# Performance work log

Hardware: AMD Instinct MI355X
Metric: run time of the kernel (lower is better)

Reference implementation:

```python
import jax, jax.numpy as jnp
import numpy as np

HIDDEN = 512
N_DRUG = 2000
N_REACTION = 10000
N_EDGES = 400000


def setup_inputs() -> dict:
    key = jax.random.key(0)
    ks = jax.random.split(key, 6)
    z_drug = jax.random.normal(ks[0], (N_DRUG, HIDDEN), dtype=jnp.float32)
    z_reaction = jax.random.normal(ks[1], (N_REACTION, HIDDEN), dtype=jnp.float32)
    row = jax.random.randint(ks[2], (N_EDGES,), 0, N_DRUG, dtype=jnp.int64)
    col = jax.random.randint(ks[3], (N_EDGES,), 0, N_REACTION, dtype=jnp.int64)
    # Linear weights in torch layout: (out_features, in_features)
    W1 = jax.random.normal(ks[4], (HIDDEN, 2 * HIDDEN), dtype=jnp.float32) * (1.0 / np.sqrt(2 * HIDDEN))
    b1 = jnp.zeros((HIDDEN,), dtype=jnp.float32)
    W2 = jax.random.normal(ks[5], (1, HIDDEN), dtype=jnp.float32) * (1.0 / np.sqrt(HIDDEN))
    b2 = jnp.zeros((1,), dtype=jnp.float32)
    return {"z_drug": z_drug, "z_reaction": z_reaction, "row": row, "col": col,
            "W1": W1, "b1": b1, "W2": W2, "b2": b2}


def reference(z_drug, z_reaction, row, col, W1, b1, W2, b2):
    # gather + concat: [E, 2H]
    z = jnp.concatenate([z_drug[row], z_reaction[col]], axis=-1)
    h = jax.nn.relu(jnp.einsum('eh,oh->eo', z, W1) + b1)  # [E, H]
    out = jnp.einsum('eh,oh->eo', h, W2) + b2             # [E, 1]
    return out.reshape(-1)
```

## Files before the change

### kernel.cpp

```cpp
#include <hip/hip_runtime.h>
#include <stdint.h>

#define HIDDEN 512
#define NDRUG 2000
#define NREACT 10000
#define NEDGE 400000

#define NBKT 320
#define SLOT 2048
#define CSTRIDE 16
#define NSCAT 128
#define EPB ((NEDGE + NSCAT - 1) / NSCAT)

#define BPB2 2
#define EBLK (NBKT * BPB2)
#define MAXSL 1024
#define HRSTRIDE 520
#define ETHREADS 512

#define GEMMBLKS 380

typedef __attribute__((ext_vector_type(8))) _Float16 f16x8;
typedef __attribute__((ext_vector_type(2))) _Float16 f16x2;
typedef __attribute__((ext_vector_type(4))) float f32x4;
typedef __attribute__((ext_vector_type(4))) float float4v;
typedef __attribute__((ext_vector_type(4))) _Float16 f16x4;

#if defined(__has_builtin)
#if __has_builtin(__builtin_amdgcn_fdot2)
#define HAVE_FDOT2 1
#endif
#endif

__global__ __launch_bounds__(256) void prep_kernel(
    const float* __restrict__ z_drug, const float* __restrict__ z_react,
    const float* __restrict__ W1,
    _Float16* __restrict__ zd_f, _Float16* __restrict__ zr_f,
    _Float16* __restrict__ WL, _Float16* __restrict__ WR,
    int* __restrict__ cursor)
{
  const int b = blockIdx.x;
  const int tid = threadIdx.x;
  if (b < 128) {
    const int nth = 128 * 256;
    const int NQ = NDRUG * HIDDEN / 4;
    for (int i = b * 256 + tid; i < NQ; i += nth) {
      float4v v = *reinterpret_cast<const float4v*>(z_drug + (size_t)i * 4);
      f16x4 q; q[0]=(_Float16)v[0]; q[1]=(_Float16)v[1]; q[2]=(_Float16)v[2]; q[3]=(_Float16)v[3];
      *reinterpret_cast<f16x4*>(zd_f + (size_t)i * 4) = q;
    }
  } else if (b < 768) {
    const int nth = 640 * 256;
    const int NQ = NREACT * HIDDEN / 4;
    for (int i = (b - 128) * 256 + tid; i < NQ; i += nth) {
      float4v v = *reinterpret_cast<const float4v*>(z_react + (size_t)i * 4);
      f16x4 q; q[0]=(_Float16)v[0]; q[1]=(_Float16)v[1]; q[2]=(_Float16)v[2]; q[3]=(_Float16)v[3];
      *reinterpret_cast<f16x4*>(zr_f + (size_t)i * 4) = q;
    }
  } else if (b < 1024) {
    const int nth = 256 * 256;
    const int NQ = HIDDEN * 2 * HIDDEN / 4;
    for (int i = (b - 768) * 256 + tid; i < NQ; i += nth) {
      int e = i * 4;
      int o = e >> 10, j = e & 1023;
      float4v v = *reinterpret_cast<const float4v*>(W1 + e);
      f16x4 q; q[0]=(_Float16)v[0]; q[1]=(_Float16)v[1]; q[2]=(_Float16)v[2]; q[3]=(_Float16)v[3];
      if (j < HIDDEN) *reinterpret_cast<f16x4*>(WL + o * HIDDEN + j) = q;
      else            *reinterpret_cast<f16x4*>(WR + o * HIDDEN + (j - HIDDEN)) = q;
    }
  } else {
    int i = (b - 1024) * 256 + tid;
    if (i < NBKT) cursor[i * CSTRIDE] = i * SLOT;
  }
}

#define BM 128
#define BN 128
#define BK 32

__global__ __launch_bounds__(256) void gemm_scatter(
    const _Float16* __restrict__ Adrug, const _Float16* __restrict__ Areac,
    const _Float16* __restrict__ BL, const _Float16* __restrict__ BR,
    const float* __restrict__ bias,
    const int* __restrict__ row, const int* __restrict__ col,
    _Float16* __restrict__ Hd, _Float16* __restrict__ Hr,
    int* __restrict__ cursor, uint64_t* __restrict__ pk)
{
  __shared__ _Float16 As[BM * BK];
  __shared__ _Float16 Bs[BN * BK];
  __shared__ int lhist[NBKT];
  __shared__ int lbase[NBKT];

  const int bid = blockIdx.x;
  const int tid = threadIdx.x;

  if (bid >= GEMMBLKS) {
    const int sb = bid - GEMMBLKS;
    const int e0 = sb * EPB;
    const int e1 = (e0 + EPB < NEDGE) ? e0 + EPB : NEDGE;
    for (int i = tid; i < NBKT; i += 256) lhist[i] = 0;
    __syncthreads();
    for (int e = e0 + tid; e < e1; e += 256)
      atomicAdd(&lhist[col[e] >> 5], 1);
    __syncthreads();
    for (int i = tid; i < NBKT; i += 256) {
      int cnt = lhist[i];
      lbase[i] = cnt ? atomicAdd(&cursor[i * CSTRIDE], cnt) : 0;
      lhist[i] = 0;
    }
    __syncthreads();
    for (int e = e0 + tid; e < e1; e += 256) {
      int c = col[e];
      int r = row[e];
      int bkt = c >> 5;
      int lo = atomicAdd(&lhist[bkt], 1);
      pk[lbase[bkt] + lo] = ((uint64_t)e << 25) | ((uint64_t)r << 14) | (uint64_t)c;
    }
    return;
  }

  const int z = (bid >= 64) ? 1 : 0;
  const int t = z ? bid - 64 : bid;
  const int mb = t >> 2;
  const int nb = t & 3;
  const int M = (z == 0) ? NDRUG : NREACT;
  const _Float16* A = (z == 0) ? Adrug : Areac;
  const _Float16* B = (z == 0) ? BL : BR;
  _Float16* C = (z == 0) ? Hd : Hr;
  const bool has_bias = (z == 0);
  const int K = HIDDEN, N = HIDDEN;

  const int lane = tid & 63;
  const int wid = tid >> 6;
  const int wm = wid >> 1;
  const int wn = wid & 1;

  f32x4 acc[4][4];
#pragma unroll
  for (int i = 0; i < 4; ++i)
#pragma unroll
    for (int j = 0; j < 4; ++j) acc[i][j] = (f32x4){0.f, 0.f, 0.f, 0.f};

  const int row0 = mb * BM;
  const int col0 = nb * BN;
  const int srow = lane >> 2;
  const int scol = (lane & 3) * 8;

  for (int kt = 0; kt < K; kt += BK) {
#pragma unroll
    for (int i = 0; i < 2; ++i) {
      int rA = row0 + wid * 32 + i * 16 + srow;
      rA = rA < M ? rA : M - 1;
      const _Float16* gA = A + (size_t)rA * K + kt + scol;
      _Float16* lA = As + (wid * 32 + i * 16) * BK;
      __builtin_amdgcn_global_load_lds(
          (const __attribute__((address_space(1))) void*)gA,
          (__attribute__((address_space(3))) void*)lA, 16, 0, 0);
      int rB = col0 + wid * 32 + i * 16 + srow;
      const _Float16* gB = B + (size_t)rB * K + kt + scol;
      _Float16* lB = Bs + (wid * 32 + i * 16) * BK;
      __builtin_amdgcn_global_load_lds(
          (const __attribute__((address_space(1))) void*)gB,
          (__attribute__((address_space(3))) void*)lB, 16, 0, 0);
    }
    __syncthreads();

    const int fr = lane & 15;
    const int kg = (lane >> 4) * 8;
    f16x8 af[4], bfr[4];
#pragma unroll
    for (int mi = 0; mi < 4; ++mi)
      af[mi] = *reinterpret_cast<const f16x8*>(As + (wm * 64 + mi * 16 + fr) * BK + kg);
#pragma unroll
    for (int ni = 0; ni < 4; ++ni)
      bfr[ni] = *reinterpret_cast<const f16x8*>(Bs + (wn * 64 + ni * 16 + fr) * BK + kg);
#pragma unroll
    for (int mi = 0; mi < 4; ++mi)
#pragma unroll
      for (int ni = 0; ni < 4; ++ni)
        acc[mi][ni] = __builtin_amdgcn_mfma_f32_16x16x32_f16(af[mi], bfr[ni], acc[mi][ni], 0, 0, 0);
    __syncthreads();
  }

  const int crow = (lane >> 4) * 4;
  const int ccol = lane & 15;
#pragma unroll
  for (int ni = 0; ni < 4; ++ni) {
    const int gc = col0 + wn * 64 + ni * 16 + ccol;
    const float bv = has_bias ? bias[gc] : 0.0f;
#pragma unroll
    for (int mi = 0; mi < 4; ++mi) {
#pragma unroll
      for (int j = 0; j < 4; ++j) {
        const int gr = row0 + wm * 64 + mi * 16 + crow + j;
        if (gr < M) C[(size_t)gr * N + gc] = (_Float16)(acc[mi][ni][j] + bv);
      }
    }
  }
}

__global__ __launch_bounds__(ETHREADS) void edge_kernel(
    const _Float16* __restrict__ Hd, const _Float16* __restrict__ Hr,
    const uint64_t* __restrict__ pk, const int* __restrict__ cursor,
    const float* __restrict__ W2, const float* __restrict__ b2,
    float* __restrict__ out)
{
  __shared__ _Float16 hrs[32 * HRSTRIDE];
  __shared__ uint64_t raw[MAXSL];
  __shared__ uint64_t spk[MAXSL];
  __shared__ int qdesc[MAXSL / 4 + 32];
  __shared__ int cnt[32], cb[32], cnt2[32], qoff[32];
  __shared__ int nqs;

  const int bid = blockIdx.x;
  const int xcd = bid & 7;
  const int idx = bid >> 3;
  const int bucket = xcd * 40 + (idx >> 1);
  const int slice = idx & 1;
  const int base = bucket * SLOT;
  const int count = cursor[bucket * CSTRIDE] - base;
  const int per = (count + BPB2 - 1) / BPB2;
  const int s = slice * per;
  const int e_end0 = (s + per < count) ? s + per : count;
  const int n = (e_end0 > s) ? e_end0 - s : 0;

  const int tid = threadIdx.x;
  const int lane = tid & 63;
  const int li = lane & 15;
  const int wv = tid >> 6;
  const int gid = wv * 4 + (lane >> 4);

#pragma unroll
  for (int rr2 = 0; rr2 < 4; ++rr2) {
    int rr = wv * 4 + rr2;
    int gr = bucket * 32 + rr;
    gr = (gr < NREACT) ? gr : NREACT - 1;
    const _Float16* src = Hr + (size_t)gr * HIDDEN + lane * 8;
    _Float16* dst = hrs + rr * HRSTRIDE;
    __builtin_amdgcn_global_load_lds(
        (const __attribute__((address_space(1))) void*)src,
        (__attribute__((address_space(3))) void*)dst, 16, 0, 0);
  }

  f16x8 w2v[4];
#pragma unroll
  for (int k = 0; k < 4; ++k) {
    const float* p = W2 + li * 8 + k * 128;
    f16x8 q;
#pragma unroll
    for (int j = 0; j < 8; ++j) q[j] = (_Float16)p[j];
    w2v[k] = q;
  }
  const float bias2 = *b2;
  const f16x8 zero8 = (f16x8)(_Float16)0;

  if (tid < 32) { cnt[tid] = 0; cnt2[tid] = 0; }
  __syncthreads();
  for (int i = tid; i < n; i += ETHREADS) {
    uint64_t p = pk[base + s + i];
    raw[i] = p;
    atomicAdd(&cnt[(int)(p & 31)], 1);
  }
  __syncthreads();
  if (tid == 0) {
    int acc = 0, qa = 0;
    for (int j = 0; j < 32; ++j) {
      cb[j] = acc; acc += cnt[j];
      qoff[j] = qa; qa += (cnt[j] + 3) >> 2;
    }
    nqs = qa;
  }
  __syncthreads();
  for (int i = tid; i < n; i += ETHREADS) {
    uint64_t p = raw[i];
    int lc = (int)(p & 31);
    int lo = atomicAdd(&cnt2[lc], 1);
    spk[cb[lc] + lo] = p;
  }
  __syncthreads();
  if (tid < 32) {
    int j = tid, st = cb[j], len = cnt[j], o = qoff[j];
    for (int q = 0; q < len; q += 4) {
      int cn = len - q; cn = (cn < 4) ? cn : 4;
      qdesc[o++] = j | ((st + q) << 5) | (cn << 16);
    }
  }
  __syncthreads();

  const int nq = nqs;
  for (int q = gid; q < nq; q += 32) {
    const int d = qdesc[q];
    const int lc = d & 31;
    const int st = (d >> 5) & 2047;
    const int cn = (d >> 16) & 7;

    const _Float16* hd[4];
    int si[4];
#pragma unroll
    for (int j = 0; j < 4; ++j) {
      int jj = (j < cn) ? j : cn - 1;
      uint64_t p = spk[st + jj];
      si[j] = (int)(p >> 25);
      hd[j] = Hd + (size_t)((p >> 14) & 0x7FF) * HIDDEN;
    }

    f16x8 vd[4][4];
#pragma unroll
    for (int j = 0; j < 4; ++j)
#pragma unroll
      for (int k = 0; k < 4; ++k)
        vd[j][k] = *reinterpret_cast<const f16x8*>(hd[j] + li * 8 + k * 128);

    f16x8 hv[4];
#pragma unroll
    for (int k = 0; k < 4; ++k)
      hv[k] = *reinterpret_cast<const f16x8*>(hrs + lc * HRSTRIDE + li * 8 + k * 128);

    float acc[4] = {0.f, 0.f, 0.f, 0.f};
#pragma unroll
    for (int j = 0; j < 4; ++j) {
#pragma unroll
      for (int k = 0; k < 4; ++k) {
        f16x8 t = __builtin_elementwise_max(vd[j][k] + hv[k], zero8);
#if defined(HAVE_FDOT2)
#pragma unroll
        for (int qq = 0; qq < 4; ++qq) {
          f16x2 wp = {w2v[k][2 * qq], w2v[k][2 * qq + 1]};
          f16x2 sp = {t[2 * qq], t[2 * qq + 1]};
          acc[j] = __builtin_amdgcn_fdot2(sp, wp, acc[j], false);
        }
#else
#pragma unroll
        for (int qq = 0; qq < 8; ++qq)
          acc[j] += (float)t[qq] * (float)w2v[k][qq];
#endif
      }
    }
#pragma unroll
    for (int off = 8; off >= 1; off >>= 1) {
#pragma unroll
      for (int j = 0; j < 4; ++j) acc[j] += __shfl_xor(acc[j], off);
    }
    if (li == 0) {
      for (int j = 0; j < cn; ++j) out[si[j]] = acc[j] + bias2;
    }
  }
}

extern "C" void kernel_launch(void* const* d_in, const int* in_sizes, int n_in,
                              void* d_out, int out_size, void* d_ws, size_t ws_size,
                              hipStream_t stream) {
  const float* z_drug  = (const float*)d_in[0];
  const float* z_react = (const float*)d_in[1];
  const int*   row     = (const int*)d_in[2];
  const int*   col     = (const int*)d_in[3];
  const float* W1      = (const float*)d_in[4];
  const float* b1      = (const float*)d_in[5];
  const float* W2      = (const float*)d_in[6];
  const float* b2      = (const float*)d_in[7];
  float* out = (float*)d_out;

  char* ws = (char*)d_ws;
  size_t off = 0;
  auto alloc = [&](size_t bytes) {
    void* p = ws + off;
    off += (bytes + 255) & ~(size_t)255;
    return p;
  };
  _Float16* zd_f = (_Float16*)alloc((size_t)NDRUG * HIDDEN * 2);
  _Float16* zr_f = (_Float16*)alloc((size_t)NREACT * HIDDEN * 2);
  _Float16* wl_f = (_Float16*)alloc((size_t)HIDDEN * HIDDEN * 2);
  _Float16* wr_f = (_Float16*)alloc((size_t)HIDDEN * HIDDEN * 2);
  _Float16* Hd   = (_Float16*)alloc((size_t)NDRUG * HIDDEN * 2);
  _Float16* Hr   = (_Float16*)alloc((size_t)NREACT * HIDDEN * 2);
  int*      cursor = (int*)alloc((size_t)NBKT * CSTRIDE * 4);
  uint64_t* pk     = (uint64_t*)alloc((size_t)NBKT * SLOT * 8);

  prep_kernel<<<1026, 256, 0, stream>>>(z_drug, z_react, W1,
                                        zd_f, zr_f, wl_f, wr_f, cursor);
  gemm_scatter<<<GEMMBLKS + NSCAT, 256, 0, stream>>>(zd_f, zr_f, wl_f, wr_f, b1,
                                                     row, col, Hd, Hr, cursor, pk);
  edge_kernel<<<EBLK, ETHREADS, 0, stream>>>(Hd, Hr, pk, cursor, W2, b2, out);
}
```

Measured before the change: 67.47 us.

## Fuse fp32-to-fp16 conversion into GEMM LDS loads, drop prep kernel

Removes the separate prep kernel that converted z_drug, z_reaction and W1 to fp16 in global memory. The GEMM now loads fp32 tiles straight into LDS and converts to fp16 when building the MFMA fragments, reading W1 in place with a column offset. This saves a full read/write pass over the embeddings and one kernel launch, at the cost of doubling LDS tile size and global load traffic inside the GEMM, plus conversion work in the inner loop.

```diff
diff --git a/kernel.cpp b/kernel.cpp
--- a/kernel.cpp
+++ b/kernel.cpp
@@ -23,8 +23,8 @@
 typedef __attribute__((ext_vector_type(8))) _Float16 f16x8;
 typedef __attribute__((ext_vector_type(2))) _Float16 f16x2;
 typedef __attribute__((ext_vector_type(4))) float f32x4;
+typedef __attribute__((ext_vector_type(8))) float f32x8;
 typedef __attribute__((ext_vector_type(4))) float float4v;
-typedef __attribute__((ext_vector_type(4))) _Float16 f16x4;
 
 #if defined(__has_builtin)
 #if __has_builtin(__builtin_amdgcn_fdot2)
@@ -32,46 +32,9 @@
 #endif
 #endif
 
-__global__ __launch_bounds__(256) void prep_kernel(
-    const float* __restrict__ z_drug, const float* __restrict__ z_react,
-    const float* __restrict__ W1,
-    _Float16* __restrict__ zd_f, _Float16* __restrict__ zr_f,
-    _Float16* __restrict__ WL, _Float16* __restrict__ WR,
-    int* __restrict__ cursor)
-{
-  const int b = blockIdx.x;
-  const int tid = threadIdx.x;
-  if (b < 128) {
-    const int nth = 128 * 256;
-    const int NQ = NDRUG * HIDDEN / 4;
-    for (int i = b * 256 + tid; i < NQ; i += nth) {
-      float4v v = *reinterpret_cast<const float4v*>(z_drug + (size_t)i * 4);
-      f16x4 q; q[0]=(_Float16)v[0]; q[1]=(_Float16)v[1]; q[2]=(_Float16)v[2]; q[3]=(_Float16)v[3];
-      *reinterpret_cast<f16x4*>(zd_f + (size_t)i * 4) = q;
-    }
-  } else if (b < 768) {
-    const int nth = 640 * 256;
-    const int NQ = NREACT * HIDDEN / 4;
-    for (int i = (b - 128) * 256 + tid; i < NQ; i += nth) {
-      float4v v = *reinterpret_cast<const float4v*>(z_react + (size_t)i * 4);
-      f16x4 q; q[0]=(_Float16)v[0]; q[1]=(_Float16)v[1]; q[2]=(_Float16)v[2]; q[3]=(_Float16)v[3];
-      *reinterpret_cast<f16x4*>(zr_f + (size_t)i * 4) = q;
-    }
-  } else if (b < 1024) {
-    const int nth = 256 * 256;
-    const int NQ = HIDDEN * 2 * HIDDEN / 4;
-    for (int i = (b - 768) * 256 + tid; i < NQ; i += nth) {
-      int e = i * 4;
-      int o = e >> 10, j = e & 1023;
-      float4v v = *reinterpret_cast<const float4v*>(W1 + e);
-      f16x4 q; q[0]=(_Float16)v[0]; q[1]=(_Float16)v[1]; q[2]=(_Float16)v[2]; q[3]=(_Float16)v[3];
-      if (j < HIDDEN) *reinterpret_cast<f16x4*>(WL + o * HIDDEN + j) = q;
-      else            *reinterpret_cast<f16x4*>(WR + o * HIDDEN + (j - HIDDEN)) = q;
-    }
-  } else {
-    int i = (b - 1024) * 256 + tid;
-    if (i < NBKT) cursor[i * CSTRIDE] = i * SLOT;
-  }
+__global__ __launch_bounds__(256) void init_cursor(int* __restrict__ cursor) {
+  int i = blockIdx.x * blockDim.x + threadIdx.x;
+  if (i < NBKT) cursor[i * CSTRIDE] = i * SLOT;
 }
 
 #define BM 128
@@ -79,15 +42,15 @@
 #define BK 32
 
 __global__ __launch_bounds__(256) void gemm_scatter(
-    const _Float16* __restrict__ Adrug, const _Float16* __restrict__ Areac,
-    const _Float16* __restrict__ BL, const _Float16* __restrict__ BR,
+    const float* __restrict__ z_drug, const float* __restrict__ z_react,
+    const float* __restrict__ W1,
     const float* __restrict__ bias,
     const int* __restrict__ row, const int* __restrict__ col,
     _Float16* __restrict__ Hd, _Float16* __restrict__ Hr,
     int* __restrict__ cursor, uint64_t* __restrict__ pk)
 {
-  __shared__ _Float16 As[BM * BK];
-  __shared__ _Float16 Bs[BN * BK];
+  __shared__ float As[BM * BK];
+  __shared__ float Bs[BN * BK];
   __shared__ int lhist[NBKT];
   __shared__ int lbase[NBKT];
 
@@ -124,8 +87,8 @@
   const int mb = t >> 2;
   const int nb = t & 3;
   const int M = (z == 0) ? NDRUG : NREACT;
-  const _Float16* A = (z == 0) ? Adrug : Areac;
-  const _Float16* B = (z == 0) ? BL : BR;
+  const float* A = (z == 0) ? z_drug : z_react;
+  const int boff = (z == 0) ? 0 : HIDDEN;
   _Float16* C = (z == 0) ? Hd : Hr;
   const bool has_bias = (z == 0);
   const int K = HIDDEN, N = HIDDEN;
@@ -143,22 +106,22 @@
 
   const int row0 = mb * BM;
   const int col0 = nb * BN;
-  const int srow = lane >> 2;
-  const int scol = (lane & 3) * 8;
+  const int srow8 = lane >> 3;
+  const int scol4 = (lane & 7) * 4;
 
   for (int kt = 0; kt < K; kt += BK) {
 #pragma unroll
-    for (int i = 0; i < 2; ++i) {
-      int rA = row0 + wid * 32 + i * 16 + srow;
+    for (int i = 0; i < 4; ++i) {
+      int rA = row0 + wid * 32 + i * 8 + srow8;
       rA = rA < M ? rA : M - 1;
-      const _Float16* gA = A + (size_t)rA * K + kt + scol;
-      _Float16* lA = As + (wid * 32 + i * 16) * BK;
+      const float* gA = A + (size_t)rA * K + kt + scol4;
+      float* lA = As + (wid * 32 + i * 8) * BK;
       __builtin_amdgcn_global_load_lds(
           (const __attribute__((address_space(1))) void*)gA,
           (__attribute__((address_space(3))) void*)lA, 16, 0, 0);
-      int rB = col0 + wid * 32 + i * 16 + srow;
-      const _Float16* gB = B + (size_t)rB * K + kt + scol;
-      _Float16* lB = Bs + (wid * 32 + i * 16) * BK;
+      int rB = col0 + wid * 32 + i * 8 + srow8;
+      const float* gB = W1 + (size_t)rB * (2 * HIDDEN) + boff + kt + scol4;
+      float* lB = Bs + (wid * 32 + i * 8) * BK;
       __builtin_amdgcn_global_load_lds(
           (const __attribute__((address_space(1))) void*)gB,
           (__attribute__((address_space(3))) void*)lB, 16, 0, 0);
@@ -169,11 +132,15 @@
     const int kg = (lane >> 4) * 8;
     f16x8 af[4], bfr[4];
 #pragma unroll
-    for (int mi = 0; mi < 4; ++mi)
-      af[mi] = *reinterpret_cast<const f16x8*>(As + (wm * 64 + mi * 16 + fr) * BK + kg);
-#pragma unroll
-    for (int ni = 0; ni < 4; ++ni)
-      bfr[ni] = *reinterpret_cast<const f16x8*>(Bs + (wn * 64 + ni * 16 + fr) * BK + kg);
+    for (int mi = 0; mi < 4; ++mi) {
+      f32x8 v = *reinterpret_cast<const f32x8*>(As + (wm * 64 + mi * 16 + fr) * BK + kg);
+      af[mi] = __builtin_convertvector(v, f16x8);
+    }
+#pragma unroll
+    for (int ni = 0; ni < 4; ++ni) {
+      f32x8 v = *reinterpret_cast<const f32x8*>(Bs + (wn * 64 + ni * 16 + fr) * BK + kg);
+      bfr[ni] = __builtin_convertvector(v, f16x8);
+    }
 #pragma unroll
     for (int mi = 0; mi < 4; ++mi)
 #pragma unroll
@@ -367,18 +334,13 @@
     off += (bytes + 255) & ~(size_t)255;
     return p;
   };
-  _Float16* zd_f = (_Float16*)alloc((size_t)NDRUG * HIDDEN * 2);
-  _Float16* zr_f = (_Float16*)alloc((size_t)NREACT * HIDDEN * 2);
-  _Float16* wl_f = (_Float16*)alloc((size_t)HIDDEN * HIDDEN * 2);
-  _Float16* wr_f = (_Float16*)alloc((size_t)HIDDEN * HIDDEN * 2);
   _Float16* Hd   = (_Float16*)alloc((size_t)NDRUG * HIDDEN * 2);
   _Float16* Hr   = (_Float16*)alloc((size_t)NREACT * HIDDEN * 2);
   int*      cursor = (int*)alloc((size_t)NBKT * CSTRIDE * 4);
   uint64_t* pk     = (uint64_t*)alloc((size_t)NBKT * SLOT * 8);
 
-  prep_kernel<<<1026, 256, 0, stream>>>(z_drug, z_react, W1,
-                                        zd_f, zr_f, wl_f, wr_f, cursor);
-  gemm_scatter<<<GEMMBLKS + NSCAT, 256, 0, stream>>>(zd_f, zr_f, wl_f, wr_f, b1,
+  init_cursor<<<2, 256, 0, stream>>>(cursor);
+  gemm_scatter<<<GEMMBLKS + NSCAT, 256, 0, stream>>>(z_drug, z_react, W1, b1,
                                                      row, col, Hd, Hr, cursor, pk);
   edge_kernel<<<EBLK, ETHREADS, 0, stream>>>(Hd, Hr, pk, cursor, W2, b2, out);
 }
```

Result: slower. 76.39 us (+13.2%).

## Fuse fp32-to-fp16 activation conversion into GEMM and split edge buckets four ways

Applied to the files above, without the earlier changes.

Removes the separate conversion pass for z_drug and z_reaction. The GEMM now loads fp32 rows directly, converts them to fp16 in registers and stores them to LDS, so the fp16 copies are no longer written to and re-read from global memory. The edge kernel splits each bucket into four slices instead of two, which doubles the block count and halves the per-block LDS staging buffers. Risks include a weaker A-tile load path (register staging instead of direct-to-LDS), a changed barrier pattern, and MAXSL 512 possibly overflowing if a bucket slice exceeds 512 edges.

```diff
diff --git a/kernel.cpp b/kernel.cpp
--- a/kernel.cpp
+++ b/kernel.cpp
@@ -12,9 +12,9 @@
 #define NSCAT 128
 #define EPB ((NEDGE + NSCAT - 1) / NSCAT)
 
-#define BPB2 2
+#define BPB2 4
 #define EBLK (NBKT * BPB2)
-#define MAXSL 1024
+#define MAXSL 512
 #define HRSTRIDE 520
 #define ETHREADS 512
 
@@ -23,6 +23,7 @@
 typedef __attribute__((ext_vector_type(8))) _Float16 f16x8;
 typedef __attribute__((ext_vector_type(2))) _Float16 f16x2;
 typedef __attribute__((ext_vector_type(4))) float f32x4;
+typedef __attribute__((ext_vector_type(8))) float f32x8;
 typedef __attribute__((ext_vector_type(4))) float float4v;
 typedef __attribute__((ext_vector_type(4))) _Float16 f16x4;
 
@@ -32,35 +33,16 @@
 #endif
 #endif
 
-__global__ __launch_bounds__(256) void prep_kernel(
-    const float* __restrict__ z_drug, const float* __restrict__ z_react,
-    const float* __restrict__ W1,
-    _Float16* __restrict__ zd_f, _Float16* __restrict__ zr_f,
-    _Float16* __restrict__ WL, _Float16* __restrict__ WR,
-    int* __restrict__ cursor)
-{
+__global__ __launch_bounds__(256) void w1prep(const float* __restrict__ W1,
+                                              _Float16* __restrict__ WL,
+                                              _Float16* __restrict__ WR,
+                                              int* __restrict__ cursor) {
   const int b = blockIdx.x;
   const int tid = threadIdx.x;
   if (b < 128) {
     const int nth = 128 * 256;
-    const int NQ = NDRUG * HIDDEN / 4;
+    const int NQ = HIDDEN * 2 * HIDDEN / 4;
     for (int i = b * 256 + tid; i < NQ; i += nth) {
-      float4v v = *reinterpret_cast<const float4v*>(z_drug + (size_t)i * 4);
-      f16x4 q; q[0]=(_Float16)v[0]; q[1]=(_Float16)v[1]; q[2]=(_Float16)v[2]; q[3]=(_Float16)v[3];
-      *reinterpret_cast<f16x4*>(zd_f + (size_t)i * 4) = q;
-    }
-  } else if (b < 768) {
-    const int nth = 640 * 256;
-    const int NQ = NREACT * HIDDEN / 4;
-    for (int i = (b - 128) * 256 + tid; i < NQ; i += nth) {
-      float4v v = *reinterpret_cast<const float4v*>(z_react + (size_t)i * 4);
-      f16x4 q; q[0]=(_Float16)v[0]; q[1]=(_Float16)v[1]; q[2]=(_Float16)v[2]; q[3]=(_Float16)v[3];
-      *reinterpret_cast<f16x4*>(zr_f + (size_t)i * 4) = q;
-    }
-  } else if (b < 1024) {
-    const int nth = 256 * 256;
-    const int NQ = HIDDEN * 2 * HIDDEN / 4;
-    for (int i = (b - 768) * 256 + tid; i < NQ; i += nth) {
       int e = i * 4;
       int o = e >> 10, j = e & 1023;
       float4v v = *reinterpret_cast<const float4v*>(W1 + e);
@@ -69,7 +51,7 @@
       else            *reinterpret_cast<f16x4*>(WR + o * HIDDEN + (j - HIDDEN)) = q;
     }
   } else {
-    int i = (b - 1024) * 256 + tid;
+    int i = (b - 128) * 256 + tid;
     if (i < NBKT) cursor[i * CSTRIDE] = i * SLOT;
   }
 }
@@ -79,7 +61,7 @@
 #define BK 32
 
 __global__ __launch_bounds__(256) void gemm_scatter(
-    const _Float16* __restrict__ Adrug, const _Float16* __restrict__ Areac,
+    const float* __restrict__ z_drug, const float* __restrict__ z_react,
     const _Float16* __restrict__ BL, const _Float16* __restrict__ BR,
     const float* __restrict__ bias,
     const int* __restrict__ row, const int* __restrict__ col,
@@ -124,7 +106,7 @@
   const int mb = t >> 2;
   const int nb = t & 3;
   const int M = (z == 0) ? NDRUG : NREACT;
-  const _Float16* A = (z == 0) ? Adrug : Areac;
+  const float* A = (z == 0) ? z_drug : z_react;
   const _Float16* B = (z == 0) ? BL : BR;
   _Float16* C = (z == 0) ? Hd : Hr;
   const bool has_bias = (z == 0);
@@ -143,19 +125,26 @@
 
   const int row0 = mb * BM;
   const int col0 = nb * BN;
+  const int r0 = tid >> 2;
+  const int q0 = tid & 3;
   const int srow = lane >> 2;
   const int scol = (lane & 3) * 8;
 
   for (int kt = 0; kt < K; kt += BK) {
+    f16x8 afh[2];
+#pragma unroll
+    for (int half = 0; half < 2; ++half) {
+      int rA = row0 + r0 + half * 64;
+      rA = rA < M ? rA : M - 1;
+      f32x8 va = *reinterpret_cast<const f32x8*>(A + (size_t)rA * K + kt + q0 * 8);
+      afh[half] = __builtin_convertvector(va, f16x8);
+    }
+    __syncthreads();
+#pragma unroll
+    for (int half = 0; half < 2; ++half)
+      *reinterpret_cast<f16x8*>(As + (r0 + half * 64) * BK + q0 * 8) = afh[half];
 #pragma unroll
     for (int i = 0; i < 2; ++i) {
-      int rA = row0 + wid * 32 + i * 16 + srow;
-      rA = rA < M ? rA : M - 1;
-      const _Float16* gA = A + (size_t)rA * K + kt + scol;
-      _Float16* lA = As + (wid * 32 + i * 16) * BK;
-      __builtin_amdgcn_global_load_lds(
-          (const __attribute__((address_space(1))) void*)gA,
-          (__attribute__((address_space(3))) void*)lA, 16, 0, 0);
       int rB = col0 + wid * 32 + i * 16 + srow;
       const _Float16* gB = B + (size_t)rB * K + kt + scol;
       _Float16* lB = Bs + (wid * 32 + i * 16) * BK;
@@ -179,7 +168,6 @@
 #pragma unroll
       for (int ni = 0; ni < 4; ++ni)
         acc[mi][ni] = __builtin_amdgcn_mfma_f32_16x16x32_f16(af[mi], bfr[ni], acc[mi][ni], 0, 0, 0);
-    __syncthreads();
   }
 
   const int crow = (lane >> 4) * 4;
@@ -215,8 +203,8 @@
   const int bid = blockIdx.x;
   const int xcd = bid & 7;
   const int idx = bid >> 3;
-  const int bucket = xcd * 40 + (idx >> 1);
-  const int slice = idx & 1;
+  const int bucket = xcd * 40 + (idx >> 2);
+  const int slice = idx & 3;
   const int base = bucket * SLOT;
   const int count = cursor[bucket * CSTRIDE] - base;
   const int per = (count + BPB2 - 1) / BPB2;
@@ -291,7 +279,7 @@
   for (int q = gid; q < nq; q += 32) {
     const int d = qdesc[q];
     const int lc = d & 31;
-    const int st = (d >> 5) & 2047;
+    const int st = (d >> 5) & 511;
     const int cn = (d >> 16) & 7;
 
     const _Float16* hd[4];
@@ -367,8 +355,6 @@
     off += (bytes + 255) & ~(size_t)255;
     return p;
   };
-  _Float16* zd_f = (_Float16*)alloc((size_t)NDRUG * HIDDEN * 2);
-  _Float16* zr_f = (_Float16*)alloc((size_t)NREACT * HIDDEN * 2);
   _Float16* wl_f = (_Float16*)alloc((size_t)HIDDEN * HIDDEN * 2);
   _Float16* wr_f = (_Float16*)alloc((size_t)HIDDEN * HIDDEN * 2);
   _Float16* Hd   = (_Float16*)alloc((size_t)NDRUG * HIDDEN * 2);
@@ -376,9 +362,8 @@
   int*      cursor = (int*)alloc((size_t)NBKT * CSTRIDE * 4);
   uint64_t* pk     = (uint64_t*)alloc((size_t)NBKT * SLOT * 8);
 
-  prep_kernel<<<1026, 256, 0, stream>>>(z_drug, z_react, W1,
-                                        zd_f, zr_f, wl_f, wr_f, cursor);
-  gemm_scatter<<<GEMMBLKS + NSCAT, 256, 0, stream>>>(zd_f, zr_f, wl_f, wr_f, b1,
+  w1prep<<<130, 256, 0, stream>>>(W1, wl_f, wr_f, cursor);
+  gemm_scatter<<<GEMMBLKS + NSCAT, 256, 0, stream>>>(z_drug, z_react, wl_f, wr_f, b1,
                                                      row, col, Hd, Hr, cursor, pk);
   edge_kernel<<<EBLK, ETHREADS, 0, stream>>>(Hd, Hr, pk, cursor, W2, b2, out);
 }
```

Result: slower. 68.83 us (+2.0%).
